# Optimization experiments

Hardware: AMD Instinct MI355X
Metric: run time of the kernel (lower is better)

Reference implementation:

```python
import jax, jax.numpy as jnp
import numpy as np

N = 500000       # total points
V = 60000        # number of voxels (segments)
XYZ_NORM = jnp.array([20.0, 20.0, 4.0], dtype=jnp.float32)
LN_EPS = 1e-3


def _ln(x, g, b):
    m = jnp.mean(x, axis=-1, keepdims=True)
    v = jnp.var(x, axis=-1, keepdims=True)
    return (x - m) * jax.lax.rsqrt(v + LN_EPS) * g + b


def _mlp_layer(x, w, b, g, be):
    # Linear -> LayerNorm -> ReLU (build_mlp in SST)
    return jax.nn.relu(_ln(x @ w + b, g, be))


def setup_inputs() -> dict:
    key = jax.random.key(0)
    ks = jax.random.split(key, 16)
    d = {
        "points": jax.random.normal(ks[0], (N, 4), jnp.float32) * 10.0,
        "features": jax.random.normal(ks[1], (N, 125), jnp.float32),
        "coors": jax.random.randint(ks[2], (N,), 0, V, jnp.int32),
        "f_cluster": jax.random.normal(ks[3], (N, 3), jnp.float32),
        "w1": jax.random.normal(ks[4], (128, 128), jnp.float32) * 0.05,
        "b1": jnp.zeros((128,), jnp.float32),
        "g1": jnp.ones((128,), jnp.float32),
        "be1": jnp.zeros((128,), jnp.float32),
        "w2": jax.random.normal(ks[5], (128, 256), jnp.float32) * 0.05,
        "b2": jnp.zeros((256,), jnp.float32),
        "g2": jnp.ones((256,), jnp.float32),
        "be2": jnp.zeros((256,), jnp.float32),
        "pw1": jax.random.normal(ks[6], (256, 256), jnp.float32) * 0.05,
        "pb1": jnp.zeros((256,), jnp.float32),
        "pg1": jnp.ones((256,), jnp.float32),
        "pbe1": jnp.zeros((256,), jnp.float32),
        "pw2": jax.random.normal(ks[7], (256, 256), jnp.float32) * 0.05,
        "pb2": jnp.zeros((256,), jnp.float32),
        "pg2": jnp.ones((256,), jnp.float32),
        "pbe2": jnp.zeros((256,), jnp.float32),
        "ow": jax.random.normal(ks[8], (256, 64), jnp.float32) * 0.05,
        "ob": jnp.zeros((64,), jnp.float32),
        "og": jnp.ones((64,), jnp.float32),
        "obe": jnp.zeros((64,), jnp.float32),
    }
    return d


def reference(points, features, coors, f_cluster,
              w1, b1, g1, be1, w2, b2, g2, be2,
              pw1, pb1, pg1, pbe1, pw2, pb2, pg2, pbe2,
              ow, ob, og, obe):
    fc = f_cluster / XYZ_NORM[None, :]
    x = jnp.concatenate([features, fc], axis=1)           # [N, 128]
    x = _mlp_layer(x, w1, b1, g1, be1)                     # [N, 128]
    x = _mlp_layer(x, w2, b2, g2, be2)                     # [N, 256]

    out_pts_feats = _mlp_layer(x, ow, ob, og, obe)         # [N, 64]

    counts = jax.ops.segment_sum(jnp.ones((x.shape[0],), x.dtype), coors,
                                 num_segments=V)           # [V]
    occ = counts > 0

    # scatter max aggregation
    agg = jax.ops.segment_max(x, coors, num_segments=V)    # [V, 256]
    agg = jnp.where(occ[:, None], agg, 0.0)
    agg = _mlp_layer(agg, pw1, pb1, pg1, pbe1)
    agg_feats = _mlp_layer(agg, pw2, pb2, pg2, pbe2)       # [V, 256]

    # scatter avg of xyz (computed in the original, used for out_coors path)
    xyz_sum = jax.ops.segment_sum(points[:, :3], coors, num_segments=V)
    cluster_xyz = xyz_sum / jnp.maximum(counts, 1.0)[:, None]
    out_coors = jnp.arange(V, dtype=jnp.int32)             # unique voxel ids
    del cluster_xyz  # not returned by the original forward

    return (out_pts_feats, agg_feats, out_coors)
```

## Files before the change

kernel.cpp:

```cpp
#include <hip/hip_runtime.h>


typedef __attribute__((ext_vector_type(4))) float f32x4;
typedef __attribute__((ext_vector_type(8))) short s16x8;
typedef __attribute__((ext_vector_type(2))) unsigned int u32x2;
typedef __attribute__((ext_vector_type(4))) unsigned int u32x4;

static constexpr int NP = 500000;
static constexpr int NV = 60000;

__device__ __forceinline__ unsigned short f2bf(float f){
  unsigned int u = __float_as_uint(f);
  u = (u + 0x7FFFu + ((u >> 16) & 1u)) >> 16;
  return (unsigned short)u;
}

__device__ __forceinline__ unsigned int cvtpk(float lo, float hi){
  unsigned int r;
  asm("v_cvt_pk_bf16_f32 %0, %1, %2" : "=v"(r) : "v"(lo), "v"(hi));
  return r;
}

__device__ __forceinline__ unsigned int pkmaxu16(unsigned int a, unsigned int b){
  unsigned int r;
  asm("v_pk_max_u16 %0, %1, %2" : "=v"(r) : "v"(a), "v"(b));
  return r;
}

__device__ __forceinline__ void pack_one(const float* __restrict__ w,
                                         unsigned short* __restrict__ dst,
                                         int K, int C, bool perm, int idx){
  int j = idx & 7, l = (idx >> 3) & 63, rest = idx >> 9;
  int kcn = K >> 5;
  int kc = rest % kcn, n = rest / kcn;
  int g = l >> 4, t = l & 15;
  int k = perm ? (kc * 32 + ((j >> 2) << 4) + g * 4 + (j & 3))
               : (kc * 32 + g * 8 + j);
  dst[idx] = f2bf(w[(size_t)k * C + n * 16 + t]);
}

__global__ void pack_hist_kernel(const float* __restrict__ w1, const float* __restrict__ w2,
                                 const float* __restrict__ ow, const float* __restrict__ pw1,
                                 const float* __restrict__ pw2,
                                 unsigned short* __restrict__ w1p, unsigned short* __restrict__ w2p,
                                 unsigned short* __restrict__ owp, unsigned short* __restrict__ pw1p,
                                 unsigned short* __restrict__ pw2p,
                                 float* __restrict__ out_coors,
                                 const int* __restrict__ coors, int* __restrict__ counts){
  int stride = gridDim.x * blockDim.x;
  const int T = 196608 + NV + NP;
  for (int i = blockIdx.x * blockDim.x + threadIdx.x; i < T; i += stride){
    if      (i < 16384)       pack_one(w1,  w1p,  128, 128, false, i);
    else if (i < 49152)       pack_one(w2,  w2p,  128, 256, true,  i - 16384);
    else if (i < 65536)       pack_one(ow,  owp,  256, 64,  true,  i - 49152);
    else if (i < 131072)      pack_one(pw1, pw1p, 256, 256, true,  i - 65536);
    else if (i < 196608)      pack_one(pw2, pw2p, 256, 256, true,  i - 131072);
    else if (i < 196608 + NV) out_coors[i - 196608] = (float)(i - 196608);
    else                      atomicAdd(&counts[coors[i - 196608 - NV]], 1);
  }
}

__global__ __launch_bounds__(1024)
void scan_kernel(const int* __restrict__ counts, int* __restrict__ cursor){
  __shared__ int part[1024];
  const int t = threadIdx.x;
  constexpr int PER = (NV + 1023) / 1024;
  int s = 0;
  for (int i = 0; i < PER; ++i){ int v = i * 1024 + t; if (v < NV) s += counts[v]; }
  part[t] = s;
  __syncthreads();
  for (int d = 1; d < 1024; d <<= 1){
    int u = (t >= d) ? part[t - d] : 0;
    __syncthreads();
    part[t] += u;
    __syncthreads();
  }
  int run = (t > 0) ? part[t - 1] : 0;
  for (int i = 0; i < PER; ++i){
    int v = i * 1024 + t;
    if (v < NV){ cursor[v] = run; run += counts[v]; }
  }
}

__global__ void scatter_kernel(const int* __restrict__ coors, int* __restrict__ cursor,
                               int* __restrict__ sidx, int* __restrict__ vsort){
  int stride = gridDim.x * blockDim.x;
  for (int i = blockIdx.x * blockDim.x + threadIdx.x; i < NP; i += stride){
    int v = coors[i];
    int p = atomicAdd(&cursor[v], 1);
    sidx[p] = i;
    vsort[p] = v;
  }
}

template<int KC, int NT>
__device__ __forceinline__ void gemm2x(const s16x8* bA, const s16x8* bB,
                                       const unsigned short* __restrict__ Wp,
                                       int lane, f32x4* dA, f32x4* dB){
#pragma unroll
  for (int n = 0; n < NT; ++n){
    f32x4 aA = {0.f,0.f,0.f,0.f}, aB = {0.f,0.f,0.f,0.f};
#pragma unroll
    for (int kc = 0; kc < KC; ++kc){
      s16x8 w = *(const s16x8*)(Wp + ((n * KC + kc) * 64 + lane) * 8);
      aA = __builtin_amdgcn_mfma_f32_16x16x32_bf16(w, bA[kc], aA, 0, 0, 0);
      aB = __builtin_amdgcn_mfma_f32_16x16x32_bf16(w, bB[kc], aB, 0, 0, 0);
    }
    dA[n] = aA; dB[n] = aB;
  }
}

template<int NT, int C>
__device__ __forceinline__ void bias_ln_relu_sw(f32x4* d0, f32x4* d1,
                                                const float* __restrict__ bias,
                                                const float* __restrict__ gam,
                                                const float* __restrict__ bet, int g){
  float s0 = 0.f, s1 = 0.f, q0 = 0.f, q1 = 0.f;
#pragma unroll
  for (int n = 0; n < NT; ++n){
    f32x4 bv = *(const f32x4*)(bias + n * 16 + g * 4);
#pragma unroll
    for (int i = 0; i < 4; ++i){
      float v0 = d0[n][i] + bv[i]; d0[n][i] = v0; s0 += v0; q0 += v0 * v0;
      float v1 = d1[n][i] + bv[i]; d1[n][i] = v1; s1 += v1; q1 += v1 * v1;
    }
  }
  s0 += __shfl_xor(s0, 16); s0 += __shfl_xor(s0, 32);
  q0 += __shfl_xor(q0, 16); q0 += __shfl_xor(q0, 32);
  s1 += __shfl_xor(s1, 16); s1 += __shfl_xor(s1, 32);
  q1 += __shfl_xor(q1, 16); q1 += __shfl_xor(q1, 32);
  float m0 = s0 * (1.f / C), m1 = s1 * (1.f / C);
  float r0 = rsqrtf(q0 * (1.f / C) - m0 * m0 + 1e-3f);
  float r1 = rsqrtf(q1 * (1.f / C) - m1 * m1 + 1e-3f);
#pragma unroll
  for (int n = 0; n < NT; ++n){
    f32x4 gv  = *(const f32x4*)(gam + n * 16 + g * 4);
    f32x4 bev = *(const f32x4*)(bet + n * 16 + g * 4);
#pragma unroll
    for (int i = 0; i < 4; ++i){
      d0[n][i] = fmaxf((d0[n][i] - m0) * r0 * gv[i] + bev[i], 0.f);
      d1[n][i] = fmaxf((d1[n][i] - m1) * r1 * gv[i] + bev[i], 0.f);
    }
  }
}

template<int NT>
__device__ __forceinline__ void to_frags(const f32x4* d, s16x8* f){
#pragma unroll
  for (int kc = 0; kc < NT / 2; ++kc){
    u32x4 t;
    t[0] = cvtpk(d[2*kc][0],   d[2*kc][1]);
    t[1] = cvtpk(d[2*kc][2],   d[2*kc][3]);
    t[2] = cvtpk(d[2*kc+1][0], d[2*kc+1][1]);
    t[3] = cvtpk(d[2*kc+1][2], d[2*kc+1][3]);
    f[kc] = __builtin_bit_cast(s16x8, t);
  }
}

__device__ __forceinline__ void load_x(const float* __restrict__ feats,
                                       const float* __restrict__ fclus,
                                       int orig, int g, s16x8* bf){
  const float* rp = feats + (size_t)orig * 125;
#pragma unroll
  for (int kc = 0; kc < 4; ++kc){
    f32x4 u0, u1;
    if (kc < 3 || g < 3){
      int q = kc * 4 + g;
      u0 = *(const f32x4*)(rp + q * 8);
      u1 = *(const f32x4*)(rp + q * 8 + 4);
    } else {
      const float* fc = fclus + (size_t)orig * 3;
      u0 = *(const f32x4*)(rp + 120);
      u1[0] = rp[124];
      u1[1] = fc[0] * 0.05f; u1[2] = fc[1] * 0.05f; u1[3] = fc[2] * 0.25f;
    }
    u32x4 t;
    t[0] = cvtpk(u0[0], u0[1]); t[1] = cvtpk(u0[2], u0[3]);
    t[2] = cvtpk(u1[0], u1[1]); t[3] = cvtpk(u1[2], u1[3]);
    bf[kc] = __builtin_bit_cast(s16x8, t);
  }
}

__device__ __forceinline__ void flush4(float* __restrict__ agg, int v, int lane,
                                       unsigned int q0, unsigned int q1, bool partial){
  float* base = agg + (size_t)v * 256 + lane * 4;
  unsigned int a0 = q0 << 16, a1 = q0 & 0xffff0000u;
  unsigned int a2 = q1 << 16, a3 = q1 & 0xffff0000u;
  if (!partial){
    f32x4 o;
    o[0] = __uint_as_float(a0); o[1] = __uint_as_float(a1);
    o[2] = __uint_as_float(a2); o[3] = __uint_as_float(a3);
    *(f32x4*)base = o;
  } else {
    unsigned int* ab = (unsigned int*)base;
    atomicMax(ab + 0, a0); atomicMax(ab + 1, a1);
    atomicMax(ab + 2, a2); atomicMax(ab + 3, a3);
  }
}

__global__ __launch_bounds__(256, 2)
void point_fused_kernel(const float* __restrict__ feats, const float* __restrict__ fclus,
                        const int* __restrict__ sidx, const int* __restrict__ vsort,
                        const unsigned short* __restrict__ w1p,
                        const unsigned short* __restrict__ w2p,
                        const unsigned short* __restrict__ owp,
                        const float* __restrict__ b1, const float* __restrict__ g1,
                        const float* __restrict__ be1,
                        const float* __restrict__ b2, const float* __restrict__ g2,
                        const float* __restrict__ be2,
                        const float* __restrict__ ob, const float* __restrict__ og,
                        const float* __restrict__ obe,
                        float* __restrict__ agg,
                        float* __restrict__ out_pts){
  __shared__ __align__(16) unsigned short tile[4][32 * 256];
  const int lane = threadIdx.x & 63;
  const int wave = threadIdx.x >> 6;
  const int g = lane >> 4, t = lane & 15;
  const int m0 = blockIdx.x * 128 + wave * 32;
  if (m0 >= NP) return;
  const int slotA = m0 + t, slotB = m0 + 16 + t;
  const int origA = sidx[slotA];
  const int origB = sidx[slotB];
  const int myv = (lane < 32) ? vsort[m0 + lane] : 0;

  s16x8 bfA[4], bfB[4];
  load_x(feats, fclus, origA, g, bfA);
  load_x(feats, fclus, origB, g, bfB);

  f32x4 d1a[8], d1b[8];
  gemm2x<4, 8>(bfA, bfB, w1p, lane, d1a, d1b);
  bias_ln_relu_sw<8, 128>(d1a, d1b, b1, g1, be1, g);
  s16x8 f2a[4], f2b[4];
  to_frags<8>(d1a, f2a); to_frags<8>(d1b, f2b);

  f32x4 d2a[16], d2b[16];
  gemm2x<4, 16>(f2a, f2b, w2p, lane, d2a, d2b);
  bias_ln_relu_sw<16, 256>(d2a, d2b, b2, g2, be2, g);
  s16x8 f3a[8], f3b[8];
  to_frags<16>(d2a, f3a); to_frags<16>(d2b, f3b);

  unsigned short* my = tile[wave];
  const int rA = t, rB = t + 16;
#pragma unroll
  for (int kc = 0; kc < 8; ++kc){
    int s = kc * 4 + g;
    int spA = (s & ~7) | ((s & 7) ^ (rA & 7));
    int spB = (s & ~7) | ((s & 7) ^ (rB & 7));
    *(s16x8*)&my[rA * 256 + spA * 8] = f3a[kc];
    *(s16x8*)&my[rB * 256 + spB * 8] = f3b[kc];
  }

  {
    f32x4 d3a[4], d3b[4];
    gemm2x<8, 4>(f3a, f3b, owp, lane, d3a, d3b);
    bias_ln_relu_sw<4, 64>(d3a, d3b, ob, og, obe, g);
#pragma unroll
    for (int n = 0; n < 4; ++n){
      *(f32x4*)(out_pts + (size_t)origA * 64 + n * 16 + g * 4) = d3a[n];
      *(f32x4*)(out_pts + (size_t)origB * 64 + n * 16 + g * 4) = d3b[n];
    }
  }

  const int vleft  = (m0 > 0) ? vsort[m0 - 1] : -1;
  const int vright = (m0 + 32 < NP) ? vsort[m0 + 32] : -1;
  const int slot = lane >> 1;
  const int half = (lane & 1) * 4;
  unsigned int q0 = 0, q1 = 0;
  int cur = __shfl(myv, 0);
  int rs = 0;
  for (int r = 0; r < 32; ++r){
    int v = __shfl(myv, r);
    if (v != cur){
      flush4(agg, cur, lane, q0, q1, rs == 0 && cur == vleft);
      q0 = 0; q1 = 0; cur = v; rs = r;
    }
    int sp = (slot & ~7) | ((slot & 7) ^ (r & 7));
    u32x2 d = *(const u32x2*)&my[r * 256 + sp * 8 + half];
    q0 = pkmaxu16(q0, d[0]);
    q1 = pkmaxu16(q1, d[1]);
  }
  flush4(agg, cur, lane, q0, q1, (rs == 0 && cur == vleft) || cur == vright);
}

__global__ __launch_bounds__(256, 2)
void vox_fused_kernel(const float* __restrict__ agg,
                      const unsigned short* __restrict__ pw1p,
                      const unsigned short* __restrict__ pw2p,
                      const float* __restrict__ pb1, const float* __restrict__ pg1,
                      const float* __restrict__ pbe1,
                      const float* __restrict__ pb2, const float* __restrict__ pg2,
                      const float* __restrict__ pbe2,
                      float* __restrict__ out_vox){
  const int lane = threadIdx.x & 63;
  const int wave = threadIdx.x >> 6;
  const int m0 = blockIdx.x * 128 + wave * 32;
  if (m0 >= NV) return;
  const int g = lane >> 4, t = lane & 15;
  const size_t mA = m0 + t, mB = m0 + 16 + t;

  s16x8 bfA[8], bfB[8];
#pragma unroll
  for (int kc = 0; kc < 8; ++kc){
    const float* pa = agg + mA * 256 + kc * 32 + g * 8;
    const float* pb = agg + mB * 256 + kc * 32 + g * 8;
    f32x4 a0 = *(const f32x4*)pa, a1 = *(const f32x4*)(pa + 4);
    f32x4 b0 = *(const f32x4*)pb, b1v = *(const f32x4*)(pb + 4);
    u32x4 ta, tb;
    ta[0] = cvtpk(a0[0], a0[1]); ta[1] = cvtpk(a0[2], a0[3]);
    ta[2] = cvtpk(a1[0], a1[1]); ta[3] = cvtpk(a1[2], a1[3]);
    tb[0] = cvtpk(b0[0], b0[1]); tb[1] = cvtpk(b0[2], b0[3]);
    tb[2] = cvtpk(b1v[0], b1v[1]); tb[3] = cvtpk(b1v[2], b1v[3]);
    bfA[kc] = __builtin_bit_cast(s16x8, ta);
    bfB[kc] = __builtin_bit_cast(s16x8, tb);
  }
  f32x4 da[16], db[16];
  gemm2x<8, 16>(bfA, bfB, pw1p, lane, da, db);
  bias_ln_relu_sw<16, 256>(da, db, pb1, pg1, pbe1, g);

  s16x8 fa[8], fb[8];
  to_frags<16>(da, fa); to_frags<16>(db, fb);

  gemm2x<8, 16>(fa, fb, pw2p, lane, da, db);
  bias_ln_relu_sw<16, 256>(da, db, pb2, pg2, pbe2, g);
#pragma unroll
  for (int n = 0; n < 16; ++n){
    *(f32x4*)(out_vox + mA * 256 + n * 16 + g * 4) = da[n];
    *(f32x4*)(out_vox + mB * 256 + n * 16 + g * 4) = db[n];
  }
}

extern "C" void kernel_launch(void* const* d_in, const int* in_sizes, int n_in,
                              void* d_out, int out_size, void* d_ws, size_t ws_size,
                              hipStream_t stream){
  const float* features  = (const float*)d_in[1];
  const int*   coors     = (const int*)  d_in[2];
  const float* f_cluster = (const float*)d_in[3];
  const float* w1  = (const float*)d_in[4];
  const float* b1  = (const float*)d_in[5];
  const float* g1  = (const float*)d_in[6];
  const float* be1 = (const float*)d_in[7];
  const float* w2  = (const float*)d_in[8];
  const float* b2  = (const float*)d_in[9];
  const float* g2  = (const float*)d_in[10];
  const float* be2 = (const float*)d_in[11];
  const float* pw1 = (const float*)d_in[12];
  const float* pb1 = (const float*)d_in[13];
  const float* pg1 = (const float*)d_in[14];
  const float* pbe1= (const float*)d_in[15];
  const float* pw2 = (const float*)d_in[16];
  const float* pb2 = (const float*)d_in[17];
  const float* pg2 = (const float*)d_in[18];
  const float* pbe2= (const float*)d_in[19];
  const float* ow  = (const float*)d_in[20];
  const float* ob  = (const float*)d_in[21];
  const float* og  = (const float*)d_in[22];
  const float* obe = (const float*)d_in[23];

  char* ws = (char*)d_ws;
  float* aggf   = (float*)(ws + 0);
  int* counts   = (int*)(ws + 61500000ull);
  int* cursor   = (int*)(ws + 61800000ull);
  int* sidx     = (int*)(ws + 62100000ull);
  int* vsort    = (int*)(ws + 64200000ull);
  unsigned short* w1p = (unsigned short*)(ws + 66300000ull);
  unsigned short* w2p = (unsigned short*)(ws + 66300000ull + 1*262144ull);
  unsigned short* owp = (unsigned short*)(ws + 66300000ull + 2*262144ull);
  unsigned short* pw1p= (unsigned short*)(ws + 66300000ull + 3*262144ull);
  unsigned short* pw2p= (unsigned short*)(ws + 66300000ull + 4*262144ull);

  float* outp      = (float*)d_out;
  float* out_pts   = outp;
  float* out_vox   = outp + 32000000;
  float* out_coors = outp + 47360000;

  hipMemsetAsync(counts, 0, (size_t)NV * sizeof(int), stream);
  hipMemsetAsync(aggf,   0, (size_t)NV * 256 * sizeof(float), stream);

  pack_hist_kernel<<<2048, 256, 0, stream>>>(w1, w2, ow, pw1, pw2,
                                             w1p, w2p, owp, pw1p, pw2p,
                                             out_coors, coors, counts);

  scan_kernel<<<1, 1024, 0, stream>>>(counts, cursor);
  scatter_kernel<<<2048, 256, 0, stream>>>(coors, cursor, sidx, vsort);

  point_fused_kernel<<<(NP + 127) / 128, 256, 0, stream>>>(
      features, f_cluster, sidx, vsort, w1p, w2p, owp,
      b1, g1, be1, b2, g2, be2, ob, og, obe, aggf, out_pts);

  vox_fused_kernel<<<(NV + 127) / 128, 256, 0, stream>>>(
      aggf, pw1p, pw2p, pb1, pg1, pbe1, pb2, pg2, pbe2, out_vox);
}
```

Before: 537.4 us.

## Keep activations packed bf16 in registers, halve LDS tile, raise occupancy

The GEMM epilogues now convert each accumulator tile to packed bf16 right after the bias add and accumulate LayerNorm statistics on the fly, then normalise in packed form. This removes the large fp32 accumulator arrays, so launch bounds can go from 2 to 3 blocks per CU. The scatter-max staging tile is halved and processed in two passes of 128 channels, and the sort index and voxel arrays are merged into one int2 array. The trade-off is extra bf16 rounding before LayerNorm, which slightly changes numerics, plus the risk of register spills at the higher occupancy target.

```diff
diff --git a/kernel.cpp b/kernel.cpp
--- a/kernel.cpp
+++ b/kernel.cpp
@@ -1,9 +1,9 @@
 #include <hip/hip_runtime.h>
 
 
+typedef __attribute__((ext_vector_type(2))) float f32x2;
 typedef __attribute__((ext_vector_type(4))) float f32x4;
 typedef __attribute__((ext_vector_type(8))) short s16x8;
-typedef __attribute__((ext_vector_type(2))) unsigned int u32x2;
 typedef __attribute__((ext_vector_type(4))) unsigned int u32x4;
 
 static constexpr int NP = 500000;
@@ -83,77 +83,12 @@
 }
 
 __global__ void scatter_kernel(const int* __restrict__ coors, int* __restrict__ cursor,
-                               int* __restrict__ sidx, int* __restrict__ vsort){
+                               int2* __restrict__ pv){
   int stride = gridDim.x * blockDim.x;
   for (int i = blockIdx.x * blockDim.x + threadIdx.x; i < NP; i += stride){
     int v = coors[i];
     int p = atomicAdd(&cursor[v], 1);
-    sidx[p] = i;
-    vsort[p] = v;
-  }
-}
-
-template<int KC, int NT>
-__device__ __forceinline__ void gemm2x(const s16x8* bA, const s16x8* bB,
-                                       const unsigned short* __restrict__ Wp,
-                                       int lane, f32x4* dA, f32x4* dB){
-#pragma unroll
-  for (int n = 0; n < NT; ++n){
-    f32x4 aA = {0.f,0.f,0.f,0.f}, aB = {0.f,0.f,0.f,0.f};
-#pragma unroll
-    for (int kc = 0; kc < KC; ++kc){
-      s16x8 w = *(const s16x8*)(Wp + ((n * KC + kc) * 64 + lane) * 8);
-      aA = __builtin_amdgcn_mfma_f32_16x16x32_bf16(w, bA[kc], aA, 0, 0, 0);
-      aB = __builtin_amdgcn_mfma_f32_16x16x32_bf16(w, bB[kc], aB, 0, 0, 0);
-    }
-    dA[n] = aA; dB[n] = aB;
-  }
-}
-
-template<int NT, int C>
-__device__ __forceinline__ void bias_ln_relu_sw(f32x4* d0, f32x4* d1,
-                                                const float* __restrict__ bias,
-                                                const float* __restrict__ gam,
-                                                const float* __restrict__ bet, int g){
-  float s0 = 0.f, s1 = 0.f, q0 = 0.f, q1 = 0.f;
-#pragma unroll
-  for (int n = 0; n < NT; ++n){
-    f32x4 bv = *(const f32x4*)(bias + n * 16 + g * 4);
-#pragma unroll
-    for (int i = 0; i < 4; ++i){
-      float v0 = d0[n][i] + bv[i]; d0[n][i] = v0; s0 += v0; q0 += v0 * v0;
-      float v1 = d1[n][i] + bv[i]; d1[n][i] = v1; s1 += v1; q1 += v1 * v1;
-    }
-  }
-  s0 += __shfl_xor(s0, 16); s0 += __shfl_xor(s0, 32);
-  q0 += __shfl_xor(q0, 16); q0 += __shfl_xor(q0, 32);
-  s1 += __shfl_xor(s1, 16); s1 += __shfl_xor(s1, 32);
-  q1 += __shfl_xor(q1, 16); q1 += __shfl_xor(q1, 32);
-  float m0 = s0 * (1.f / C), m1 = s1 * (1.f / C);
-  float r0 = rsqrtf(q0 * (1.f / C) - m0 * m0 + 1e-3f);
-  float r1 = rsqrtf(q1 * (1.f / C) - m1 * m1 + 1e-3f);
-#pragma unroll
-  for (int n = 0; n < NT; ++n){
-    f32x4 gv  = *(const f32x4*)(gam + n * 16 + g * 4);
-    f32x4 bev = *(const f32x4*)(bet + n * 16 + g * 4);
-#pragma unroll
-    for (int i = 0; i < 4; ++i){
-      d0[n][i] = fmaxf((d0[n][i] - m0) * r0 * gv[i] + bev[i], 0.f);
-      d1[n][i] = fmaxf((d1[n][i] - m1) * r1 * gv[i] + bev[i], 0.f);
-    }
-  }
-}
-
-template<int NT>
-__device__ __forceinline__ void to_frags(const f32x4* d, s16x8* f){
-#pragma unroll
-  for (int kc = 0; kc < NT / 2; ++kc){
-    u32x4 t;
-    t[0] = cvtpk(d[2*kc][0],   d[2*kc][1]);
-    t[1] = cvtpk(d[2*kc][2],   d[2*kc][3]);
-    t[2] = cvtpk(d[2*kc+1][0], d[2*kc+1][1]);
-    t[3] = cvtpk(d[2*kc+1][2], d[2*kc+1][3]);
-    f[kc] = __builtin_bit_cast(s16x8, t);
+    pv[p] = make_int2(i, v);
   }
 }
 
@@ -181,26 +116,82 @@
   }
 }
 
-__device__ __forceinline__ void flush4(float* __restrict__ agg, int v, int lane,
-                                       unsigned int q0, unsigned int q1, bool partial){
-  float* base = agg + (size_t)v * 256 + lane * 4;
-  unsigned int a0 = q0 << 16, a1 = q0 & 0xffff0000u;
-  unsigned int a2 = q1 << 16, a3 = q1 & 0xffff0000u;
+template<int KC, int NT>
+__device__ __forceinline__ void gemm_pack(const unsigned int* pa_in, const unsigned int* pb_in,
+                                          const unsigned short* __restrict__ Wp,
+                                          const float* __restrict__ bias,
+                                          int lane, int g,
+                                          unsigned int* pa, unsigned int* pb,
+                                          float& sA, float& qA, float& sB, float& qB){
+#pragma unroll
+  for (int n = 0; n < NT; ++n){
+    f32x4 aA = {0.f,0.f,0.f,0.f}, aB = {0.f,0.f,0.f,0.f};
+#pragma unroll
+    for (int kc = 0; kc < KC; ++kc){
+      s16x8 w = *(const s16x8*)(Wp + ((n * KC + kc) * 64 + lane) * 8);
+      s16x8 fa = __builtin_bit_cast(s16x8, *(const u32x4*)&pa_in[4 * kc]);
+      s16x8 fb = __builtin_bit_cast(s16x8, *(const u32x4*)&pb_in[4 * kc]);
+      aA = __builtin_amdgcn_mfma_f32_16x16x32_bf16(w, fa, aA, 0, 0, 0);
+      aB = __builtin_amdgcn_mfma_f32_16x16x32_bf16(w, fb, aB, 0, 0, 0);
+    }
+    f32x4 bv = *(const f32x4*)(bias + n * 16 + g * 4);
+#pragma unroll
+    for (int i = 0; i < 4; ++i){
+      aA[i] += bv[i]; sA += aA[i]; qA += aA[i] * aA[i];
+      aB[i] += bv[i]; sB += aB[i]; qB += aB[i] * aB[i];
+    }
+    pa[2*n] = cvtpk(aA[0], aA[1]); pa[2*n+1] = cvtpk(aA[2], aA[3]);
+    pb[2*n] = cvtpk(aB[0], aB[1]); pb[2*n+1] = cvtpk(aB[2], aB[3]);
+  }
+}
+
+template<int NT, int C>
+__device__ __forceinline__ void ln_pack(unsigned int* pa, unsigned int* pb,
+                                        const float* __restrict__ gam,
+                                        const float* __restrict__ bet, int g,
+                                        float sA, float qA, float sB, float qB){
+  sA += __shfl_xor(sA, 16); sA += __shfl_xor(sA, 32);
+  qA += __shfl_xor(qA, 16); qA += __shfl_xor(qA, 32);
+  sB += __shfl_xor(sB, 16); sB += __shfl_xor(sB, 32);
+  qB += __shfl_xor(qB, 16); qB += __shfl_xor(qB, 32);
+  float mA = sA * (1.f / C), mB = sB * (1.f / C);
+  float rA = rsqrtf(qA * (1.f / C) - mA * mA + 1e-3f);
+  float rB = rsqrtf(qB * (1.f / C) - mB * mB + 1e-3f);
+#pragma unroll
+  for (int n = 0; n < NT; ++n){
+    f32x4 gv  = *(const f32x4*)(gam + n * 16 + g * 4);
+    f32x4 bev = *(const f32x4*)(bet + n * 16 + g * 4);
+#pragma unroll
+    for (int h = 0; h < 2; ++h){
+      unsigned int ua = pa[2*n+h], ub = pb[2*n+h];
+      float a0 = __uint_as_float(ua << 16), a1 = __uint_as_float(ua & 0xffff0000u);
+      float b0 = __uint_as_float(ub << 16), b1 = __uint_as_float(ub & 0xffff0000u);
+      a0 = fmaxf((a0 - mA) * rA * gv[2*h]   + bev[2*h],   0.f);
+      a1 = fmaxf((a1 - mA) * rA * gv[2*h+1] + bev[2*h+1], 0.f);
+      b0 = fmaxf((b0 - mB) * rB * gv[2*h]   + bev[2*h],   0.f);
+      b1 = fmaxf((b1 - mB) * rB * gv[2*h+1] + bev[2*h+1], 0.f);
+      pa[2*n+h] = cvtpk(a0, a1);
+      pb[2*n+h] = cvtpk(b0, b1);
+    }
+  }
+}
+
+__device__ __forceinline__ void flush2(float* __restrict__ agg, int v, int c0,
+                                       unsigned int q, bool partial){
+  float* base = agg + (size_t)v * 256 + c0;
+  unsigned int a0 = q << 16, a1 = q & 0xffff0000u;
   if (!partial){
-    f32x4 o;
-    o[0] = __uint_as_float(a0); o[1] = __uint_as_float(a1);
-    o[2] = __uint_as_float(a2); o[3] = __uint_as_float(a3);
-    *(f32x4*)base = o;
+    f32x2 o; o[0] = __uint_as_float(a0); o[1] = __uint_as_float(a1);
+    *(f32x2*)base = o;
   } else {
     unsigned int* ab = (unsigned int*)base;
     atomicMax(ab + 0, a0); atomicMax(ab + 1, a1);
-    atomicMax(ab + 2, a2); atomicMax(ab + 3, a3);
-  }
-}
-
-__global__ __launch_bounds__(256, 2)
+  }
+}
+
+__global__ __launch_bounds__(256, 3)
 void point_fused_kernel(const float* __restrict__ feats, const float* __restrict__ fclus,
-                        const int* __restrict__ sidx, const int* __restrict__ vsort,
+                        const int2* __restrict__ pv,
                         const unsigned short* __restrict__ w1p,
                         const unsigned short* __restrict__ w2p,
                         const unsigned short* __restrict__ owp,
@@ -212,74 +203,117 @@
                         const float* __restrict__ obe,
                         float* __restrict__ agg,
                         float* __restrict__ out_pts){
-  __shared__ __align__(16) unsigned short tile[4][32 * 256];
+  __shared__ __align__(16) unsigned short tile[4][32 * 128];
   const int lane = threadIdx.x & 63;
   const int wave = threadIdx.x >> 6;
   const int g = lane >> 4, t = lane & 15;
   const int m0 = blockIdx.x * 128 + wave * 32;
   if (m0 >= NP) return;
-  const int slotA = m0 + t, slotB = m0 + 16 + t;
-  const int origA = sidx[slotA];
-  const int origB = sidx[slotB];
-  const int myv = (lane < 32) ? vsort[m0 + lane] : 0;
+  const int2 pA = pv[m0 + t];
+  const int2 pB = pv[m0 + 16 + t];
+  const int origA = pA.x, origB = pB.x;
+  const int myv = pv[m0 + (lane & 31)].y;
 
   s16x8 bfA[4], bfB[4];
   load_x(feats, fclus, origA, g, bfA);
   load_x(feats, fclus, origB, g, bfB);
 
-  f32x4 d1a[8], d1b[8];
-  gemm2x<4, 8>(bfA, bfB, w1p, lane, d1a, d1b);
-  bias_ln_relu_sw<8, 128>(d1a, d1b, b1, g1, be1, g);
-  s16x8 f2a[4], f2b[4];
-  to_frags<8>(d1a, f2a); to_frags<8>(d1b, f2b);
-
-  f32x4 d2a[16], d2b[16];
-  gemm2x<4, 16>(f2a, f2b, w2p, lane, d2a, d2b);
-  bias_ln_relu_sw<16, 256>(d2a, d2b, b2, g2, be2, g);
-  s16x8 f3a[8], f3b[8];
-  to_frags<16>(d2a, f3a); to_frags<16>(d2b, f3b);
-
-  unsigned short* my = tile[wave];
-  const int rA = t, rB = t + 16;
-#pragma unroll
-  for (int kc = 0; kc < 8; ++kc){
-    int s = kc * 4 + g;
-    int spA = (s & ~7) | ((s & 7) ^ (rA & 7));
-    int spB = (s & ~7) | ((s & 7) ^ (rB & 7));
-    *(s16x8*)&my[rA * 256 + spA * 8] = f3a[kc];
-    *(s16x8*)&my[rB * 256 + spB * 8] = f3b[kc];
+  unsigned int p1a[16], p1b[16];
+  {
+    float sA = 0, qA = 0, sB = 0, qB = 0;
+    gemm_pack<4, 8>((const unsigned int*)bfA, (const unsigned int*)bfB, w1p, b1,
+                    lane, g, p1a, p1b, sA, qA, sB, qB);
+    ln_pack<8, 128>(p1a, p1b, g1, be1, g, sA, qA, sB, qB);
+  }
+
+  unsigned int p2a[32], p2b[32];
+  {
+    float sA = 0, qA = 0, sB = 0, qB = 0;
+    gemm_pack<4, 16>(p1a, p1b, w2p, b2, lane, g, p2a, p2b, sA, qA, sB, qB);
+    ln_pack<16, 256>(p2a, p2b, g2, be2, g, sA, qA, sB, qB);
   }
 
   {
     f32x4 d3a[4], d3b[4];
-    gemm2x<8, 4>(f3a, f3b, owp, lane, d3a, d3b);
-    bias_ln_relu_sw<4, 64>(d3a, d3b, ob, og, obe, g);
 #pragma unroll
     for (int n = 0; n < 4; ++n){
-      *(f32x4*)(out_pts + (size_t)origA * 64 + n * 16 + g * 4) = d3a[n];
-      *(f32x4*)(out_pts + (size_t)origB * 64 + n * 16 + g * 4) = d3b[n];
-    }
-  }
-
-  const int vleft  = (m0 > 0) ? vsort[m0 - 1] : -1;
-  const int vright = (m0 + 32 < NP) ? vsort[m0 + 32] : -1;
-  const int slot = lane >> 1;
-  const int half = (lane & 1) * 4;
-  unsigned int q0 = 0, q1 = 0;
-  int cur = __shfl(myv, 0);
-  int rs = 0;
-  for (int r = 0; r < 32; ++r){
-    int v = __shfl(myv, r);
-    if (v != cur){
-      flush4(agg, cur, lane, q0, q1, rs == 0 && cur == vleft);
-      q0 = 0; q1 = 0; cur = v; rs = r;
-    }
-    int sp = (slot & ~7) | ((slot & 7) ^ (r & 7));
-    u32x2 d = *(const u32x2*)&my[r * 256 + sp * 8 + half];
-    q0 = pkmaxu16(q0, d[0]);
-    q1 = pkmaxu16(q1, d[1]);
-  }
-  flush4(agg, cur, lane, q0, q1, (rs == 0 && cur == vleft) || cur == vright);
+      f32x4 aA = {0.f,0.f,0.f,0.f}, aB = {0.f,0.f,0.f,0.f};
+#pragma unroll
+      for (int kc = 0; kc < 8; ++kc){
+        s16x8 w = *(const s16x8*)(owp + ((n * 8 + kc) * 64 + lane) * 8);
+        s16x8 fa = __builtin_bit_cast(s16x8, *(const u32x4*)&p2a[4 * kc]);
+        s16x8 fb = __builtin_bit_cast(s16x8, *(const u32x4*)&p2b[4 * kc]);
+        aA = __builtin_amdgcn_mfma_f32_16x16x32_bf16(w, fa, aA, 0, 0, 0);
+        aB = __builtin_amdgcn_mfma_f32_16x16x32_bf16(w, fb, aB, 0, 0, 0);
+      }
+      d3a[n] = aA; d3b[n] = aB;
+    }
+    float sA = 0, qA = 0, sB = 0, qB = 0;
+#pragma unroll
+    for (int n = 0; n < 4; ++n){
+      f32x4 bv = *(const f32x4*)(ob + n * 16 + g * 4);
+#pragma unroll
+      for (int i = 0; i < 4; ++i){
+        d3a[n][i] += bv[i]; sA += d3a[n][i]; qA += d3a[n][i] * d3a[n][i];
+        d3b[n][i] += bv[i]; sB += d3b[n][i]; qB += d3b[n][i] * d3b[n][i];
+      }
+    }
+    sA += __shfl_xor(sA, 16); sA += __shfl_xor(sA, 32);
+    qA += __shfl_xor(qA, 16); qA += __shfl_xor(qA, 32);
+    sB += __shfl_xor(sB, 16); sB += __shfl_xor(sB, 32);
+    qB += __shfl_xor(qB, 16); qB += __shfl_xor(qB, 32);
+    float mA = sA * (1.f/64), mB = sB * (1.f/64);
+    float rA = rsqrtf(qA * (1.f/64) - mA * mA + 1e-3f);
+    float rB = rsqrtf(qB * (1.f/64) - mB * mB + 1e-3f);
+#pragma unroll
+    for (int n = 0; n < 4; ++n){
+      f32x4 gv  = *(const f32x4*)(og  + n * 16 + g * 4);
+      f32x4 bev = *(const f32x4*)(obe + n * 16 + g * 4);
+      f32x4 oA, oB;
+#pragma unroll
+      for (int i = 0; i < 4; ++i){
+        oA[i] = fmaxf((d3a[n][i] - mA) * rA * gv[i] + bev[i], 0.f);
+        oB[i] = fmaxf((d3b[n][i] - mB) * rB * gv[i] + bev[i], 0.f);
+      }
+      *(f32x4*)(out_pts + (size_t)origA * 64 + n * 16 + g * 4) = oA;
+      *(f32x4*)(out_pts + (size_t)origB * 64 + n * 16 + g * 4) = oB;
+    }
+  }
+
+  unsigned short* my = tile[wave];
+  const int vleft  = (m0 > 0) ? pv[m0 - 1].y : -1;
+  const int vright = (m0 + 32 < NP) ? pv[m0 + 32].y : -1;
+  const int rA = t, rB = t + 16;
+  const int slot = lane >> 2;
+  const int off  = (lane & 3) * 2;
+
+#pragma unroll
+  for (int pass = 0; pass < 2; ++pass){
+#pragma unroll
+    for (int kcp = 0; kcp < 4; ++kcp){
+      int s = kcp * 4 + g;
+      int spA = (s & ~7) | ((s & 7) ^ (rA & 7));
+      int spB = (s & ~7) | ((s & 7) ^ (rB & 7));
+      int kc = pass * 4 + kcp;
+      *(s16x8*)&my[rA * 128 + spA * 8] = __builtin_bit_cast(s16x8, *(const u32x4*)&p2a[4 * kc]);
+      *(s16x8*)&my[rB * 128 + spB * 8] = __builtin_bit_cast(s16x8, *(const u32x4*)&p2b[4 * kc]);
+    }
+    const int c0 = pass * 128 + lane * 2;
+    unsigned int q = 0;
+    int cur = __shfl(myv, 0);
+    int rs = 0;
+#pragma unroll
+    for (int r = 0; r < 32; ++r){
+      int v = __shfl(myv, r);
+      if (v != cur){
+        flush2(agg, cur, c0, q, rs == 0 && cur == vleft);
+        q = 0; cur = v; rs = r;
+      }
+      int sp = (slot & ~7) | ((slot & 7) ^ (r & 7));
+      q = pkmaxu16(q, *(const unsigned int*)&my[r * 128 + sp * 8 + off]);
+    }
+    flush2(agg, cur, c0, q, (rs == 0 && cur == vleft) || cur == vright);
+  }
 }
 
 __global__ __launch_bounds__(256, 2)
@@ -298,34 +332,69 @@
   const int g = lane >> 4, t = lane & 15;
   const size_t mA = m0 + t, mB = m0 + 16 + t;
 
-  s16x8 bfA[8], bfB[8];
+  unsigned int ba[32], bb[32];
 #pragma unroll
   for (int kc = 0; kc < 8; ++kc){
     const float* pa = agg + mA * 256 + kc * 32 + g * 8;
     const float* pb = agg + mB * 256 + kc * 32 + g * 8;
     f32x4 a0 = *(const f32x4*)pa, a1 = *(const f32x4*)(pa + 4);
     f32x4 b0 = *(const f32x4*)pb, b1v = *(const f32x4*)(pb + 4);
-    u32x4 ta, tb;
-    ta[0] = cvtpk(a0[0], a0[1]); ta[1] = cvtpk(a0[2], a0[3]);
-    ta[2] = cvtpk(a1[0], a1[1]); ta[3] = cvtpk(a1[2], a1[3]);
-    tb[0] = cvtpk(b0[0], b0[1]); tb[1] = cvtpk(b0[2], b0[3]);
-    tb[2] = cvtpk(b1v[0], b1v[1]); tb[3] = cvtpk(b1v[2], b1v[3]);
-    bfA[kc] = __builtin_bit_cast(s16x8, ta);
-    bfB[kc] = __builtin_bit_cast(s16x8, tb);
-  }
+    ba[4*kc]   = cvtpk(a0[0], a0[1]); ba[4*kc+1] = cvtpk(a0[2], a0[3]);
+    ba[4*kc+2] = cvtpk(a1[0], a1[1]); ba[4*kc+3] = cvtpk(a1[2], a1[3]);
+    bb[4*kc]   = cvtpk(b0[0], b0[1]); bb[4*kc+1] = cvtpk(b0[2], b0[3]);
+    bb[4*kc+2] = cvtpk(b1v[0], b1v[1]); bb[4*kc+3] = cvtpk(b1v[2], b1v[3]);
+  }
+
+  unsigned int pa1[32], pb1a[32];
+  {
+    float sA = 0, qA = 0, sB = 0, qB = 0;
+    gemm_pack<8, 16>(ba, bb, pw1p, pb1, lane, g, pa1, pb1a, sA, qA, sB, qB);
+    ln_pack<16, 256>(pa1, pb1a, pg1, pbe1, g, sA, qA, sB, qB);
+  }
+
   f32x4 da[16], db[16];
-  gemm2x<8, 16>(bfA, bfB, pw1p, lane, da, db);
-  bias_ln_relu_sw<16, 256>(da, db, pb1, pg1, pbe1, g);
-
-  s16x8 fa[8], fb[8];
-  to_frags<16>(da, fa); to_frags<16>(db, fb);
-
-  gemm2x<8, 16>(fa, fb, pw2p, lane, da, db);
-  bias_ln_relu_sw<16, 256>(da, db, pb2, pg2, pbe2, g);
 #pragma unroll
   for (int n = 0; n < 16; ++n){
-    *(f32x4*)(out_vox + mA * 256 + n * 16 + g * 4) = da[n];
-    *(f32x4*)(out_vox + mB * 256 + n * 16 + g * 4) = db[n];
+    f32x4 aA = {0.f,0.f,0.f,0.f}, aB = {0.f,0.f,0.f,0.f};
+#pragma unroll
+    for (int kc = 0; kc < 8; ++kc){
+      s16x8 w = *(const s16x8*)(pw2p + ((n * 8 + kc) * 64 + lane) * 8);
+      s16x8 fa = __builtin_bit_cast(s16x8, *(const u32x4*)&pa1[4 * kc]);
+      s16x8 fb = __builtin_bit_cast(s16x8, *(const u32x4*)&pb1a[4 * kc]);
+      aA = __builtin_amdgcn_mfma_f32_16x16x32_bf16(w, fa, aA, 0, 0, 0);
+      aB = __builtin_amdgcn_mfma_f32_16x16x32_bf16(w, fb, aB, 0, 0, 0);
+    }
+    da[n] = aA; db[n] = aB;
+  }
+  float sA = 0, qA = 0, sB = 0, qB = 0;
+#pragma unroll
+  for (int n = 0; n < 16; ++n){
+    f32x4 bv = *(const f32x4*)(pb2 + n * 16 + g * 4);
+#pragma unroll
+    for (int i = 0; i < 4; ++i){
+      da[n][i] += bv[i]; sA += da[n][i]; qA += da[n][i] * da[n][i];
+      db[n][i] += bv[i]; sB += db[n][i]; qB += db[n][i] * db[n][i];
+    }
+  }
+  sA += __shfl_xor(sA, 16); sA += __shfl_xor(sA, 32);
+  qA += __shfl_xor(qA, 16); qA += __shfl_xor(qA, 32);
+  sB += __shfl_xor(sB, 16); sB += __shfl_xor(sB, 32);
+  qB += __shfl_xor(qB, 16); qB += __shfl_xor(qB, 32);
+  float mAs = sA * (1.f/256), mBs = sB * (1.f/256);
+  float rAs = rsqrtf(qA * (1.f/256) - mAs * mAs + 1e-3f);
+  float rBs = rsqrtf(qB * (1.f/256) - mBs * mBs + 1e-3f);
+#pragma unroll
+  for (int n = 0; n < 16; ++n){
+    f32x4 gv  = *(const f32x4*)(pg2  + n * 16 + g * 4);
+    f32x4 bev = *(const f32x4*)(pbe2 + n * 16 + g * 4);
+    f32x4 oA, oB;
+#pragma unroll
+    for (int i = 0; i < 4; ++i){
+      oA[i] = fmaxf((da[n][i] - mAs) * rAs * gv[i] + bev[i], 0.f);
+      oB[i] = fmaxf((db[n][i] - mBs) * rBs * gv[i] + bev[i], 0.f);
+    }
+    *(f32x4*)(out_vox + mA * 256 + n * 16 + g * 4) = oA;
+    *(f32x4*)(out_vox + mB * 256 + n * 16 + g * 4) = oB;
   }
 }
 
@@ -360,8 +429,7 @@
   float* aggf   = (float*)(ws + 0);
   int* counts   = (int*)(ws + 61500000ull);
   int* cursor   = (int*)(ws + 61800000ull);
-  int* sidx     = (int*)(ws + 62100000ull);
-  int* vsort    = (int*)(ws + 64200000ull);
+  int2* pv      = (int2*)(ws + 62100000ull);
   unsigned short* w1p = (unsigned short*)(ws + 66300000ull);
   unsigned short* w2p = (unsigned short*)(ws + 66300000ull + 1*262144ull);
   unsigned short* owp = (unsigned short*)(ws + 66300000ull + 2*262144ull);
@@ -381,10 +449,10 @@
                                              out_coors, coors, counts);
 
   scan_kernel<<<1, 1024, 0, stream>>>(counts, cursor);
-  scatter_kernel<<<2048, 256, 0, stream>>>(coors, cursor, sidx, vsort);
+  scatter_kernel<<<2048, 256, 0, stream>>>(coors, cursor, pv);
 
   point_fused_kernel<<<(NP + 127) / 128, 256, 0, stream>>>(
-      features, f_cluster, sidx, vsort, w1p, w2p, owp,
+      features, f_cluster, pv, w1p, w2p, owp,
       b1, g1, be1, b2, g2, be2, ob, og, obe, aggf, out_pts);
 
   vox_fused_kernel<<<(NV + 127) / 128, 256, 0, stream>>>(
```

Result: slower. 555.2 us (+3.3%).

## Pre-convert features to bf16 in sorted order during scatter; pack index and voxel pairs

Applied to the files above, without the earlier changes.

The scatter kernel now also reads each point's feature row and f_cluster values, converts them to bf16, and writes a 128-element row at the point's sorted slot. The fused point kernel then loads contiguous bf16 rows instead of gathering fp32 rows through an index. The separate sidx and vsort arrays are merged into one int2 array. This halves the bytes the MLP kernel reads and removes its indirect gather, but it adds a 128MB write and read-back through the workspace. The scatter kernel's per-thread row reads are also poorly coalesced.

```diff
diff --git a/kernel.cpp b/kernel.cpp
--- a/kernel.cpp
+++ b/kernel.cpp
@@ -82,14 +82,37 @@
   }
 }
 
-__global__ void scatter_kernel(const int* __restrict__ coors, int* __restrict__ cursor,
-                               int* __restrict__ sidx, int* __restrict__ vsort){
+__global__ void scatter_prep_kernel(const int* __restrict__ coors, int* __restrict__ cursor,
+                                    const float* __restrict__ feats,
+                                    const float* __restrict__ fclus,
+                                    int2* __restrict__ pv,
+                                    unsigned int* __restrict__ x0u){
   int stride = gridDim.x * blockDim.x;
   for (int i = blockIdx.x * blockDim.x + threadIdx.x; i < NP; i += stride){
     int v = coors[i];
     int p = atomicAdd(&cursor[v], 1);
-    sidx[p] = i;
-    vsort[p] = v;
+    pv[p] = make_int2(i, v);
+    const float* rp = feats + (size_t)i * 125;
+    unsigned int* dst = x0u + (size_t)p * 64;
+#pragma unroll
+    for (int k = 0; k < 15; ++k){
+      f32x4 a = *(const f32x4*)(rp + k * 8);
+      f32x4 b = *(const f32x4*)(rp + k * 8 + 4);
+      u32x4 o;
+      o[0] = cvtpk(a[0], a[1]); o[1] = cvtpk(a[2], a[3]);
+      o[2] = cvtpk(b[0], b[1]); o[3] = cvtpk(b[2], b[3]);
+      *(u32x4*)(dst + k * 4) = o;
+    }
+    {
+      f32x4 a = *(const f32x4*)(rp + 120);
+      const float* fc = fclus + (size_t)i * 3;
+      u32x4 o;
+      o[0] = cvtpk(a[0], a[1]);
+      o[1] = cvtpk(a[2], a[3]);
+      o[2] = cvtpk(rp[124], fc[0] * 0.05f);
+      o[3] = cvtpk(fc[1] * 0.05f, fc[2] * 0.25f);
+      *(u32x4*)(dst + 60) = o;
+    }
   }
 }
 
@@ -154,30 +177,6 @@
     t[2] = cvtpk(d[2*kc+1][0], d[2*kc+1][1]);
     t[3] = cvtpk(d[2*kc+1][2], d[2*kc+1][3]);
     f[kc] = __builtin_bit_cast(s16x8, t);
-  }
-}
-
-__device__ __forceinline__ void load_x(const float* __restrict__ feats,
-                                       const float* __restrict__ fclus,
-                                       int orig, int g, s16x8* bf){
-  const float* rp = feats + (size_t)orig * 125;
-#pragma unroll
-  for (int kc = 0; kc < 4; ++kc){
-    f32x4 u0, u1;
-    if (kc < 3 || g < 3){
-      int q = kc * 4 + g;
-      u0 = *(const f32x4*)(rp + q * 8);
-      u1 = *(const f32x4*)(rp + q * 8 + 4);
-    } else {
-      const float* fc = fclus + (size_t)orig * 3;
-      u0 = *(const f32x4*)(rp + 120);
-      u1[0] = rp[124];
-      u1[1] = fc[0] * 0.05f; u1[2] = fc[1] * 0.05f; u1[3] = fc[2] * 0.25f;
-    }
-    u32x4 t;
-    t[0] = cvtpk(u0[0], u0[1]); t[1] = cvtpk(u0[2], u0[3]);
-    t[2] = cvtpk(u1[0], u1[1]); t[3] = cvtpk(u1[2], u1[3]);
-    bf[kc] = __builtin_bit_cast(s16x8, t);
   }
 }
 
@@ -199,8 +198,8 @@
 }
 
 __global__ __launch_bounds__(256, 2)
-void point_fused_kernel(const float* __restrict__ feats, const float* __restrict__ fclus,
-                        const int* __restrict__ sidx, const int* __restrict__ vsort,
+void point_fused_kernel(const unsigned short* __restrict__ x0,
+                        const int2* __restrict__ pv,
                         const unsigned short* __restrict__ w1p,
                         const unsigned short* __restrict__ w2p,
                         const unsigned short* __restrict__ owp,
@@ -219,13 +218,17 @@
   const int m0 = blockIdx.x * 128 + wave * 32;
   if (m0 >= NP) return;
   const int slotA = m0 + t, slotB = m0 + 16 + t;
-  const int origA = sidx[slotA];
-  const int origB = sidx[slotB];
-  const int myv = (lane < 32) ? vsort[m0 + lane] : 0;
+  const int2 pA = pv[slotA];
+  const int2 pB = pv[slotB];
+  const int origA = pA.x, origB = pB.x;
+  const int myv = pv[m0 + (lane & 31)].y;
 
   s16x8 bfA[4], bfB[4];
-  load_x(feats, fclus, origA, g, bfA);
-  load_x(feats, fclus, origB, g, bfB);
+#pragma unroll
+  for (int kc = 0; kc < 4; ++kc){
+    bfA[kc] = *(const s16x8*)(x0 + (size_t)slotA * 128 + (kc * 4 + g) * 8);
+    bfB[kc] = *(const s16x8*)(x0 + (size_t)slotB * 128 + (kc * 4 + g) * 8);
+  }
 
   f32x4 d1a[8], d1b[8];
   gemm2x<4, 8>(bfA, bfB, w1p, lane, d1a, d1b);
@@ -261,8 +264,8 @@
     }
   }
 
-  const int vleft  = (m0 > 0) ? vsort[m0 - 1] : -1;
-  const int vright = (m0 + 32 < NP) ? vsort[m0 + 32] : -1;
+  const int vleft  = (m0 > 0) ? pv[m0 - 1].y : -1;
+  const int vright = (m0 + 32 < NP) ? pv[m0 + 32].y : -1;
   const int slot = lane >> 1;
   const int half = (lane & 1) * 4;
   unsigned int q0 = 0, q1 = 0;
@@ -360,13 +363,14 @@
   float* aggf   = (float*)(ws + 0);
   int* counts   = (int*)(ws + 61500000ull);
   int* cursor   = (int*)(ws + 61800000ull);
-  int* sidx     = (int*)(ws + 62100000ull);
-  int* vsort    = (int*)(ws + 64200000ull);
-  unsigned short* w1p = (unsigned short*)(ws + 66300000ull);
-  unsigned short* w2p = (unsigned short*)(ws + 66300000ull + 1*262144ull);
-  unsigned short* owp = (unsigned short*)(ws + 66300000ull + 2*262144ull);
-  unsigned short* pw1p= (unsigned short*)(ws + 66300000ull + 3*262144ull);
-  unsigned short* pw2p= (unsigned short*)(ws + 66300000ull + 4*262144ull);
+  int2* pv      = (int2*)(ws + 62100000ull);
+  unsigned int* x0u = (unsigned int*)(ws + 66200000ull);
+  unsigned short* x0 = (unsigned short*)x0u;
+  unsigned short* w1p = (unsigned short*)(ws + 195000000ull);
+  unsigned short* w2p = (unsigned short*)(ws + 195000000ull + 1*262144ull);
+  unsigned short* owp = (unsigned short*)(ws + 195000000ull + 2*262144ull);
+  unsigned short* pw1p= (unsigned short*)(ws + 195000000ull + 3*262144ull);
+  unsigned short* pw2p= (unsigned short*)(ws + 195000000ull + 4*262144ull);
 
   float* outp      = (float*)d_out;
   float* out_pts   = outp;
@@ -381,10 +385,12 @@
                                              out_coors, coors, counts);
 
   scan_kernel<<<1, 1024, 0, stream>>>(counts, cursor);
-  scatter_kernel<<<2048, 256, 0, stream>>>(coors, cursor, sidx, vsort);
+
+  scatter_prep_kernel<<<2048, 256, 0, stream>>>(coors, cursor, features, f_cluster,
+                                                pv, x0u);
 
   point_fused_kernel<<<(NP + 127) / 128, 256, 0, stream>>>(
-      features, f_cluster, sidx, vsort, w1p, w2p, owp,
+      x0, pv, w1p, w2p, owp,
       b1, g1, be1, b2, g2, be2, ob, og, obe, aggf, out_pts);
 
   vox_fused_kernel<<<(NV + 127) / 128, 256, 0, stream>>>(
```

Result: slower. 604.3 us (+12.5%).
